# Kernel tuning notes

Hardware: AMD Instinct MI355X
Metric: run time of the kernel (lower is better)

## Reference

```python
import jax, jax.numpy as jnp
import numpy as np

A, B, K = 8192, 8192, 10

def setup_inputs() -> dict:
    key = jax.random.key(0)
    k1, k2, k3 = jax.random.split(key, 3)
    W = jax.random.uniform(k1, (A, B), dtype=jnp.float32)      # similarity weights (a,b)
    P_l = jax.random.uniform(k2, (A, K), dtype=jnp.float32)    # left cluster probs (a,k)
    P_r = jax.random.uniform(k3, (B, K), dtype=jnp.float32)    # right cluster probs (b,k)
    clusters_p = jnp.ones((K,), dtype=jnp.float32) / K         # nn.Parameter ones(k)/k
    return {"W": W, "P_l": P_l, "P_r": P_r, "clusters_p": clusters_p}

def reference(W, P_l, P_r, clusters_p):
    # Original math: sum_{a,b,k} W[a,b] * (P_l[a,k] + P_r[b,k] - 2*P_l[a,k]*P_r[b,k]) / clusters_p[k]
    # Decomposes exactly (no (a,b,k) intermediate):
    row_sum = W.sum(axis=1)                 # (a,)
    col_sum = W.sum(axis=0)                 # (b,)
    term_l = row_sum @ P_l                  # (k,)  sum_a rowsum[a] * P_l[a,k]
    term_r = col_sum @ P_r                  # (k,)  sum_b colsum[b] * P_r[b,k]
    WPr = W @ P_r                           # (a,k)
    cross = jnp.sum(P_l * WPr, axis=0)      # (k,)  diag(P_l^T W P_r)
    per_cluster = term_l + term_r - 2.0 * cross
    return jnp.sum(per_cluster / clusters_p)
```

## Files before the change

### kernel.cpp

```cpp
#include <hip/hip_runtime.h>


constexpr int K     = 10;
constexpr int REC   = 12;
constexpr int TM    = 32;
constexpr int BLOCK = 1024;
constexpr int COLS  = BLOCK * 2;
constexpr int P     = 4;

typedef float f2 __attribute__((ext_vector_type(2)));

__global__ void prcut_prep(const float* __restrict__ Pl,
                           const float* __restrict__ cp,
                           float* __restrict__ rec,
                           float* __restrict__ out, int A)
{
    const int a = blockIdx.x * blockDim.x + threadIdx.x;
    if (a == 0) out[0] = 0.0f;
    if (a >= A) return;
    float la = 0.0f;
    float r[REC];
#pragma unroll
    for (int k = 0; k < K; ++k) {
        const float p = Pl[(size_t)a * K + k];
        la = fmaf(p, 1.0f / cp[k], la);
        r[1 + k] = -2.0f * p;
    }
    r[0] = la;
    r[11] = 0.0f;
#pragma unroll
    for (int k = 0; k < REC; ++k) rec[(size_t)a * REC + k] = r[k];
}

__global__ __launch_bounds__(BLOCK, 8) void prcut_main(
    const float* __restrict__ W,
    const float* __restrict__ Pr,
    const float* __restrict__ cp,
    const float* __restrict__ rec,
    float* __restrict__ out,
    int Bn)
{
    const int c0 = blockIdx.x * COLS + threadIdx.x * 2;
    const int a0 = blockIdx.y * TM;

    float pr[2][K];
    float rs[2];
#pragma unroll
    for (int j = 0; j < 2; ++j) {
        const float* p = Pr + (size_t)(c0 + j) * K;
        float s = 0.0f;
#pragma unroll
        for (int k = 0; k < K; ++k) {
            const float v = p[k] * (1.0f / cp[k]);
            pr[j][k] = v;
            s += v;
        }
        rs[j] = s;
    }

    const float* wp  = W + (size_t)a0 * Bn + c0;
    const float* wld = wp + (size_t)P * Bn;

    f2 wbuf[P];
#pragma unroll
    for (int i = 0; i < P; ++i)
        wbuf[i] = __builtin_nontemporal_load(
            reinterpret_cast<const f2*>(wp + (size_t)i * Bn));

    float acc = 0.0f;
    const float* rp = rec + (size_t)a0 * REC;

#pragma unroll 4
    for (int r = 0; r < TM - P; ++r) {
        const float la = rp[0];
        float d0 = la + rs[0];
        float d1 = la + rs[1];
#pragma unroll
        for (int k = 0; k < K; ++k) {
            const float q = rp[1 + k];
            d0 = fmaf(q, pr[0][k], d0);
            d1 = fmaf(q, pr[1][k], d1);
        }
        rp += REC;

        const int slot = r & (P - 1);
        const f2 w = wbuf[slot];
        wbuf[slot] = __builtin_nontemporal_load(
            reinterpret_cast<const f2*>(wld));
        wld += Bn;

        acc = fmaf(w.x, d0, fmaf(w.y, d1, acc));
    }

#pragma unroll
    for (int r = TM - P; r < TM; ++r) {
        const float la = rp[0];
        float d0 = la + rs[0];
        float d1 = la + rs[1];
#pragma unroll
        for (int k = 0; k < K; ++k) {
            const float q = rp[1 + k];
            d0 = fmaf(q, pr[0][k], d0);
            d1 = fmaf(q, pr[1][k], d1);
        }
        rp += REC;

        const f2 w = wbuf[r & (P - 1)];
        acc = fmaf(w.x, d0, fmaf(w.y, d1, acc));
    }

#pragma unroll
    for (int off = 32; off > 0; off >>= 1)
        acc += __shfl_down(acc, off, 64);

    __shared__ float wsum[BLOCK / 64];
    const int lane = threadIdx.x & 63;
    const int wid  = threadIdx.x >> 6;
    if (lane == 0) wsum[wid] = acc;
    __syncthreads();

    if (threadIdx.x == 0) {
        float s = 0.0f;
#pragma unroll
        for (int i = 0; i < BLOCK / 64; ++i) s += wsum[i];
        atomicAdd(out, s);
    }
}

extern "C" void kernel_launch(void* const* d_in, const int* in_sizes, int n_in,
                              void* d_out, int out_size, void* d_ws, size_t ws_size,
                              hipStream_t stream) {
    const float* W  = (const float*)d_in[0];
    const float* Pl = (const float*)d_in[1];
    const float* Pr = (const float*)d_in[2];
    const float* cp = (const float*)d_in[3];
    float* out = (float*)d_out;
    float* rec = (float*)d_ws;

    const int Kn = in_sizes[3];
    const int A  = in_sizes[1] / Kn;
    const int B  = in_sizes[2] / Kn;

    prcut_prep<<<(A + 255) / 256, 256, 0, stream>>>(Pl, cp, rec, out, A);

    dim3 grid(B / COLS, A / TM);
    prcut_main<<<grid, BLOCK, 0, stream>>>(W, Pr, cp, rec, out, B);
}
```

Baseline: 349.9 us.

## Widen per-thread tile to four columns and stage row records in LDS

Each thread now handles four adjacent columns with 16-byte W loads, and the block shrinks to 512 threads with a shallower prefetch depth. The 32 row records are loaded once per block into shared memory and read back as vector loads, replacing repeated global reads. This is meant to cut per-element load instructions and amortize the row-record reads over more columns, at the cost of more registers for Pr values and a block-wide barrier.

```diff
diff --git a/kernel.cpp b/kernel.cpp
--- a/kernel.cpp
+++ b/kernel.cpp
@@ -4,11 +4,11 @@
 constexpr int K     = 10;
 constexpr int REC   = 12;
 constexpr int TM    = 32;
-constexpr int BLOCK = 1024;
-constexpr int COLS  = BLOCK * 2;
-constexpr int P     = 4;
+constexpr int BLOCK = 512;
+constexpr int COLS  = BLOCK * 4;
+constexpr int P     = 2;
 
-typedef float f2 __attribute__((ext_vector_type(2)));
+typedef float f4 __attribute__((ext_vector_type(4)));
 
 __global__ void prcut_prep(const float* __restrict__ Pl,
                            const float* __restrict__ cp,
@@ -26,13 +26,13 @@
         la = fmaf(p, 1.0f / cp[k], la);
         r[1 + k] = -2.0f * p;
     }
-    r[0] = la;
+    r[0]  = la;
     r[11] = 0.0f;
 #pragma unroll
     for (int k = 0; k < REC; ++k) rec[(size_t)a * REC + k] = r[k];
 }
 
-__global__ __launch_bounds__(BLOCK, 8) void prcut_main(
+__global__ __launch_bounds__(BLOCK, 6) void prcut_main(
     const float* __restrict__ W,
     const float* __restrict__ Pr,
     const float* __restrict__ cp,
@@ -40,13 +40,16 @@
     float* __restrict__ out,
     int Bn)
 {
-    const int c0 = blockIdx.x * COLS + threadIdx.x * 2;
+    __shared__ f4 lrec[TM * REC / 4];
+    const int t  = threadIdx.x;
     const int a0 = blockIdx.y * TM;
+    if (t < TM * REC) ((float*)lrec)[t] = rec[(size_t)a0 * REC + t];
 
-    float pr[2][K];
-    float rs[2];
+    const int c0 = blockIdx.x * COLS + t * 4;
+    float pr[4][K];
+    float rs[4];
 #pragma unroll
-    for (int j = 0; j < 2; ++j) {
+    for (int j = 0; j < 4; ++j) {
         const float* p = Pr + (size_t)(c0 + j) * K;
         float s = 0.0f;
 #pragma unroll
@@ -57,56 +60,72 @@
         }
         rs[j] = s;
     }
+    __syncthreads();
 
     const float* wp  = W + (size_t)a0 * Bn + c0;
     const float* wld = wp + (size_t)P * Bn;
 
-    f2 wbuf[P];
+    f4 wbuf[P];
 #pragma unroll
     for (int i = 0; i < P; ++i)
         wbuf[i] = __builtin_nontemporal_load(
-            reinterpret_cast<const f2*>(wp + (size_t)i * Bn));
+            reinterpret_cast<const f4*>(wp + (size_t)i * Bn));
 
     float acc = 0.0f;
-    const float* rp = rec + (size_t)a0 * REC;
 
 #pragma unroll 4
     for (int r = 0; r < TM - P; ++r) {
-        const float la = rp[0];
-        float d0 = la + rs[0];
-        float d1 = la + rs[1];
+        const f4 qa = lrec[r * 3 + 0];
+        const f4 qb = lrec[r * 3 + 1];
+        const f4 qc = lrec[r * 3 + 2];
+        const float la = qa.x;
+        const float qv[K] = {qa.y, qa.z, qa.w, qb.x, qb.y,
+                             qb.z, qb.w, qc.x, qc.y, qc.z};
+
+        float d[4];
+#pragma unroll
+        for (int j = 0; j < 4; ++j) d[j] = la + rs[j];
 #pragma unroll
         for (int k = 0; k < K; ++k) {
-            const float q = rp[1 + k];
-            d0 = fmaf(q, pr[0][k], d0);
-            d1 = fmaf(q, pr[1][k], d1);
+#pragma unroll
+            for (int j = 0; j < 4; ++j) d[j] = fmaf(qv[k], pr[j][k], d[j]);
         }
-        rp += REC;
 
         const int slot = r & (P - 1);
-        const f2 w = wbuf[slot];
+        const f4 w = wbuf[slot];
         wbuf[slot] = __builtin_nontemporal_load(
-            reinterpret_cast<const f2*>(wld));
+            reinterpret_cast<const f4*>(wld));
         wld += Bn;
 
-        acc = fmaf(w.x, d0, fmaf(w.y, d1, acc));
+        acc = fmaf(w.x, d[0], acc);
+        acc = fmaf(w.y, d[1], acc);
+        acc = fmaf(w.z, d[2], acc);
+        acc = fmaf(w.w, d[3], acc);
     }
 
 #pragma unroll
     for (int r = TM - P; r < TM; ++r) {
-        const float la = rp[0];
-        float d0 = la + rs[0];
-        float d1 = la + rs[1];
+        const f4 qa = lrec[r * 3 + 0];
+        const f4 qb = lrec[r * 3 + 1];
+        const f4 qc = lrec[r * 3 + 2];
+        const float la = qa.x;
+        const float qv[K] = {qa.y, qa.z, qa.w, qb.x, qb.y,
+                             qb.z, qb.w, qc.x, qc.y, qc.z};
+
+        float d[4];
+#pragma unroll
+        for (int j = 0; j < 4; ++j) d[j] = la + rs[j];
 #pragma unroll
         for (int k = 0; k < K; ++k) {
-            const float q = rp[1 + k];
-            d0 = fmaf(q, pr[0][k], d0);
-            d1 = fmaf(q, pr[1][k], d1);
+#pragma unroll
+            for (int j = 0; j < 4; ++j) d[j] = fmaf(qv[k], pr[j][k], d[j]);
         }
-        rp += REC;
 
-        const f2 w = wbuf[r & (P - 1)];
-        acc = fmaf(w.x, d0, fmaf(w.y, d1, acc));
+        const f4 w = wbuf[r & (P - 1)];
+        acc = fmaf(w.x, d[0], acc);
+        acc = fmaf(w.y, d[1], acc);
+        acc = fmaf(w.z, d[2], acc);
+        acc = fmaf(w.w, d[3], acc);
     }
 
 #pragma unroll
@@ -114,12 +133,12 @@
         acc += __shfl_down(acc, off, 64);
 
     __shared__ float wsum[BLOCK / 64];
-    const int lane = threadIdx.x & 63;
-    const int wid  = threadIdx.x >> 6;
+    const int lane = t & 63;
+    const int wid  = t >> 6;
     if (lane == 0) wsum[wid] = acc;
     __syncthreads();
 
-    if (threadIdx.x == 0) {
+    if (t == 0) {
         float s = 0.0f;
 #pragma unroll
         for (int i = 0; i < BLOCK / 64; ++i) s += wsum[i];
```

Result: no change. 349.7 us (-0.0%).
